# Kernel optimization log

Hardware: AMD Instinct MI355X
Metric: run time of the kernel (lower is better)

The kernel has to match this reference:

```python
import jax, jax.numpy as jnp
import numpy as np

B, C, T, H = 16, 128, 128, 128


def setup_inputs() -> dict:
    key = jax.random.key(0)
    ks = jax.random.split(key, 9)
    inp = {
        "food_relation": jax.random.normal(ks[0], (B, C, H), jnp.float32),
        "thorn_relation": jax.random.normal(ks[1], (B, C, T, H), jnp.float32),
        "clone": jax.random.normal(ks[2], (B, C, H), jnp.float32),
        "clone_relation": jax.random.normal(ks[3], (B, C, C, H), jnp.float32),
        "thorn_mask": jax.random.randint(ks[4], (B, T), 0, 2, jnp.int32),
        "clone_mask": jax.random.randint(ks[5], (B, C), 0, 2, jnp.int32),
        # MLP(layer_num=1) == Linear(in, h) + activation (ReLU)
        "W_thorn": jax.random.normal(ks[6], (2 * H, H), jnp.float32) / np.sqrt(2 * H),
        "b_thorn": jnp.zeros((H,), jnp.float32),
        "W_clone": jax.random.normal(ks[7], (3 * H, H), jnp.float32) / np.sqrt(3 * H),
        "b_clone": jnp.zeros((H,), jnp.float32),
        "W_agg": jax.random.normal(ks[8], (4 * H, H), jnp.float32) / np.sqrt(4 * H),
        "b_agg": jnp.zeros((H,), jnp.float32),
    }
    return inp


def reference(food_relation, thorn_relation, clone, clone_relation,
              thorn_mask, clone_mask,
              W_thorn, b_thorn, W_clone, b_clone, W_agg, b_agg):
    b, c, h = clone.shape
    t = thorn_relation.shape[2]
    tm = thorn_mask.astype(clone.dtype)[:, None, :, None]  # (b,1,t,1)
    cm = clone_mask.astype(clone.dtype)[:, None, :, None]  # (b,1,c,1)

    # thorn branch: MLP(concat([clone_i, thorn_rel_ij], -1))
    # == clone @ W[:h] (broadcast over t) + rel @ W[h:], avoiding the big concat
    x = ((clone @ W_thorn[:h])[:, :, None, :]
         + jnp.einsum('bcth,hk->bctk', thorn_relation, W_thorn[h:])
         + b_thorn)  # (b,c,t,h)
    thorn_agg = jnp.max(jax.nn.relu(x) * tm, axis=2)  # (b,c,h)

    # clone branch: MLP(concat([clone_i, clone_j, clone_rel_ij], -1))
    y = ((clone @ W_clone[:h])[:, :, None, :]
         + (clone @ W_clone[h:2 * h])[:, None, :, :]
         + jnp.einsum('bcdh,hk->bcdk', clone_relation, W_clone[2 * h:])
         + b_clone)  # (b,c,c,h)
    clone_agg = jnp.max(jax.nn.relu(y) * cm, axis=2)  # (b,c,h)

    agg = jnp.concatenate([clone, food_relation, thorn_agg, clone_agg], axis=-1)  # (b,c,4h)
    return clone + jax.nn.relu(agg @ W_agg + b_agg)
```

## Files before the change

kernel.cpp:

```cpp
#include <hip/hip_runtime.h>

#define BB 16
#define CC 128
#define TT 128
#define HH 128
#define BC (BB*CC)

typedef __attribute__((ext_vector_type(8))) short bf16x8;
typedef __attribute__((ext_vector_type(4))) float f32x4;

__device__ __forceinline__ unsigned short f2bf(float f) {
  union { float f; unsigned u; } v; v.f = f;
  unsigned u = v.u;
  u += 0x7FFFu + ((u >> 16) & 1u);
  return (unsigned short)(u >> 16);
}

__device__ __forceinline__ bf16x8 pack8(f32x4 a, f32x4 b) {
  bf16x8 r;
  r[0] = (short)f2bf(a[0]); r[1] = (short)f2bf(a[1]);
  r[2] = (short)f2bf(a[2]); r[3] = (short)f2bf(a[3]);
  r[4] = (short)f2bf(b[0]); r[5] = (short)f2bf(b[1]);
  r[6] = (short)f2bf(b[2]); r[7] = (short)f2bf(b[3]);
  return r;
}

__device__ __forceinline__ float bf2f(unsigned short u) {
  union { unsigned u; float f; } v; v.u = ((unsigned)u) << 16; return v.f;
}

__global__ __launch_bounds__(256) void prep_kernel(
    const float* __restrict__ Wt, const float* __restrict__ Wc, const float* __restrict__ Wa,
    const float* __restrict__ clone, const float* __restrict__ food,
    const float* __restrict__ bt, const float* __restrict__ bcl,
    const int* __restrict__ tmask, const int* __restrict__ cmask,
    unsigned short* __restrict__ W2sw, unsigned short* __restrict__ Wcsw,
    unsigned short* __restrict__ WaggT,
    float* __restrict__ cpt, float* __restrict__ cp1, float* __restrict__ cj2,
    unsigned short* __restrict__ agg,
    int* __restrict__ tidx, int* __restrict__ tcnt,
    int* __restrict__ cidx, int* __restrict__ ccnt) {
  const int blk = blockIdx.x, tid = threadIdx.x;
  if (blk < 48) {
    int i = blk * 256 + tid;
    if (i < 2048) {
      int f = i >> 6, l = i & 63;
      int kt = f >> 3, n = f & 7;
      int ncol = n * 16 + (l & 15);
      int k0 = kt * 32 + (l >> 4) * 8;
      unsigned short o[8];
      #pragma unroll
      for (int e = 0; e < 8; ++e) o[e] = f2bf(Wt[(128 + k0 + e) * 128 + ncol]);
      *(uint4*)&W2sw[i * 8] = *(uint4*)o;
    } else if (i < 4096) {
      int j = i - 2048;
      int f = j >> 6, l = j & 63;
      int kt = f >> 3, n = f & 7;
      int ncol = n * 16 + (l & 15);
      int k0 = kt * 32 + (l >> 4) * 8;
      unsigned short o[8];
      #pragma unroll
      for (int e = 0; e < 8; ++e) o[e] = f2bf(Wc[(256 + k0 + e) * 128 + ncol]);
      *(uint4*)&Wcsw[j * 8] = *(uint4*)o;
    } else {
      int j = i - 4096;
      int n = j >> 6, k0 = (j & 63) * 8;
      unsigned short o[8];
      #pragma unroll
      for (int e = 0; e < 8; ++e) o[e] = f2bf(Wa[(k0 + e) * 128 + n]);
      *(uint4*)&WaggT[n * 512 + k0] = *(uint4*)o;
    }
  } else if (blk < 304) {
    const int bc0 = (blk - 48) * 8;
    __shared__ float cl[8][128];
    for (int i = tid; i < 1024; i += 256) cl[i >> 7][i & 127] = clone[bc0 * 128 + i];
    __syncthreads();
    const int k = tid & 127, r0 = (tid >> 7) * 4;
    float s1[4], s2[4], s3[4];
    #pragma unroll
    for (int r = 0; r < 4; ++r) { s1[r] = bt[k]; s2[r] = bcl[k]; s3[r] = 0.f; }
    #pragma unroll 4
    for (int h = 0; h < 128; ++h) {
      float w1 = Wt[h * 128 + k], w2 = Wc[h * 128 + k], w3 = Wc[(128 + h) * 128 + k];
      #pragma unroll
      for (int r = 0; r < 4; ++r) {
        float c = cl[r0 + r][h];
        s1[r] = fmaf(c, w1, s1[r]);
        s2[r] = fmaf(c, w2, s2[r]);
        s3[r] = fmaf(c, w3, s3[r]);
      }
    }
    #pragma unroll
    for (int r = 0; r < 4; ++r) {
      cpt[(bc0 + r0 + r) * 128 + k] = s1[r];
      cp1[(bc0 + r0 + r) * 128 + k] = s2[r];
      cj2[(bc0 + r0 + r) * 128 + k] = s3[r];
    }
    for (int i = tid; i < 1024; i += 256) {
      int r = i >> 7, kk = i & 127;
      agg[(size_t)(bc0 + r) * 512 + kk]       = f2bf(cl[r][kk]);
      agg[(size_t)(bc0 + r) * 512 + 128 + kk] = f2bf(food[bc0 * 128 + i]);
    }
  } else {
    if (tid < 32) {
      int b = tid >> 1, which = tid & 1;
      const int* m = which ? cmask : tmask;
      int* idx = which ? cidx : tidx;
      int c = 0;
      for (int i = 0; i < 128; ++i)
        if (m[b * 128 + i]) idx[b * 128 + c++] = i;
      if (which) ccnt[b] = c; else tcnt[b] = c;
    }
  }
}

__global__ __launch_bounds__(512, 4) void branch9(
    const float* __restrict__ trel, const float* __restrict__ crel,
    const float* __restrict__ cpt, const float* __restrict__ cp1,
    const float* __restrict__ cj2,
    const int* __restrict__ tidx, const int* __restrict__ tcnt,
    const int* __restrict__ cidx, const int* __restrict__ ccnt,
    const uint4* __restrict__ W2sw, const uint4* __restrict__ Wcsw,
    unsigned short* __restrict__ agg) {
  __shared__ uint4 Wlds[32 * 64];
  __shared__ unsigned short cj2l[128][130];
  __shared__ float redbuf[2][8][128];
  __shared__ int idxl[128];
  __shared__ float biasl[8][128];

  const bool isClone = blockIdx.x < 256;
  const int tileIdx = blockIdx.x & 255;
  const float* __restrict__ rel     = isClone ? crel  : trel;
  const float* __restrict__ biasrow = isClone ? cp1   : cpt;
  const int*   __restrict__ idxg    = isClone ? cidx  : tidx;
  const uint4* __restrict__ Wsw     = isClone ? Wcsw  : W2sw;
  const int aggoff = isClone ? 384 : 256;

  const int tid = threadIdx.x;
  const int wave = tid >> 6, lane = tid & 63;
  const int l16 = lane & 15, lk = lane >> 4;
  const int bc0 = tileIdx << 3;
  const int b = bc0 >> 7;
  const int cnt = (isClone ? ccnt : tcnt)[b];
  const int cl  = cnt > 0 ? cnt : 1;
  const bool active = (wave * 16) < cnt;

  for (int i = tid; i < 2048; i += 512) Wlds[i] = Wsw[i];
  if (tid < 128) idxl[tid] = idxg[b * 128 + tid];
  #pragma unroll
  for (int i = 0; i < 2; ++i) {
    int q = i * 512 + tid;
    biasl[q >> 7][q & 127] = biasrow[bc0 * 128 + q];
  }
  if (isClone) {
    const float* cg = cj2 + (size_t)b * 128 * 128;
    for (int i = tid; i < 2048; i += 512) {
      int r = i >> 4, c8 = (i & 15) * 8;
      f32x4 a0 = *(const f32x4*)(cg + r * 128 + c8);
      f32x4 a1 = *(const f32x4*)(cg + r * 128 + c8 + 4);
      bf16x8 p = pack8(a0, a1);
      #pragma unroll
      for (int e = 0; e < 8; ++e) cj2l[c8 + e][r] = (unsigned short)p[e];
    }
  }
  __syncthreads();

  int rsel = wave * 16 + l16; if (rsel >= cl) rsel = cl - 1;
  const int row = active ? idxl[rsel] : 0;
  const float* R0 = rel + ((size_t)bc0 * 128 + row) * 128 + lk * 8;

  int rowj[4];
  if (isClone) {
    #pragma unroll
    for (int j = 0; j < 4; ++j) {
      int rs = wave * 16 + lk * 4 + j; if (rs >= cl) rs = cl - 1;
      rowj[j] = idxl[rs];
    }
  }

  f32x4 pf[4][2];
  if (active) {
    #pragma unroll
    for (int kt = 0; kt < 4; ++kt) {
      pf[kt][0] = *(const f32x4*)(R0 + kt * 32);
      pf[kt][1] = *(const f32x4*)(R0 + kt * 32 + 4);
    }
  }

  for (int t = 0; t < 8; ++t) {
    const int bc = bc0 + t;

    if (active) {
      bf16x8 afr[4];
      #pragma unroll
      for (int kt = 0; kt < 4; ++kt) afr[kt] = pack8(pf[kt][0], pf[kt][1]);

      if (t < 7) {
        const float* Rn = R0 + (size_t)(t + 1) * 16384;
        #pragma unroll
        for (int kt = 0; kt < 4; ++kt) {
          pf[kt][0] = *(const f32x4*)(Rn + kt * 32);
          pf[kt][1] = *(const f32x4*)(Rn + kt * 32 + 4);
        }
      }

      f32x4 acc[8];
      #pragma unroll
      for (int n = 0; n < 8; ++n) acc[n] = (f32x4){0.f, 0.f, 0.f, 0.f};
      #pragma unroll
      for (int kt = 0; kt < 4; ++kt) {
        #pragma unroll
        for (int n = 0; n < 8; ++n) {
          bf16x8 bfr = *(const bf16x8*)&Wlds[(kt * 8 + n) * 64 + lane];
          acc[n] = __builtin_amdgcn_mfma_f32_16x16x32_bf16(afr[kt], bfr, acc[n], 0, 0, 0);
        }
      }

      #pragma unroll
      for (int n = 0; n < 8; ++n) {
        const int col = n * 16 + l16;
        float bias = biasl[t][col];
        float m0 = 0.f;
        if (isClone) {
          #pragma unroll
          for (int j = 0; j < 4; ++j) {
            float x = acc[n][j] + bias + bf2f(cj2l[col][rowj[j]]);
            m0 = fmaxf(m0, fmaxf(x, 0.f));
          }
        } else {
          #pragma unroll
          for (int j = 0; j < 4; ++j)
            m0 = fmaxf(m0, fmaxf(acc[n][j] + bias, 0.f));
        }
        float v = fmaxf(m0, __shfl_xor(m0, 16));
        v = fmaxf(v, __shfl_xor(v, 32));
        if (lane < 16) redbuf[t & 1][wave][col] = v;
      }
    } else {
      if (lane < 16) {
        #pragma unroll
        for (int n = 0; n < 8; ++n) redbuf[t & 1][wave][n * 16 + lane] = 0.f;
      }
    }
    __syncthreads();
    if (tid < 128) {
      float v = redbuf[t & 1][0][tid];
      #pragma unroll
      for (int w2 = 1; w2 < 8; ++w2) v = fmaxf(v, redbuf[t & 1][w2][tid]);
      agg[(size_t)bc * 512 + aggoff + tid] = f2bf(v);
    }
  }
}

__global__ __launch_bounds__(256) void final_kernel(
    const unsigned short* __restrict__ agg, const unsigned short* __restrict__ WaggT,
    const float* __restrict__ clone, const float* __restrict__ bagg,
    float* __restrict__ out) {
  const int tid = threadIdx.x;
  const int wave = tid >> 6, lane = tid & 63;
  const int l16 = lane & 15, lk = lane >> 4;
  const int mrow = blockIdx.x * 16;

  f32x4 acc[2];
  acc[0] = (f32x4){0.f, 0.f, 0.f, 0.f};
  acc[1] = (f32x4){0.f, 0.f, 0.f, 0.f};
  #pragma unroll
  for (int kt = 0; kt < 16; ++kt) {
    bf16x8 a = *(const bf16x8*)(agg + (size_t)(mrow + l16) * 512 + kt * 32 + lk * 8);
    #pragma unroll
    for (int nn = 0; nn < 2; ++nn) {
      int ncol = (wave * 2 + nn) * 16 + l16;
      bf16x8 bfr = *(const bf16x8*)(WaggT + (size_t)ncol * 512 + kt * 32 + lk * 8);
      acc[nn] = __builtin_amdgcn_mfma_f32_16x16x32_bf16(a, bfr, acc[nn], 0, 0, 0);
    }
  }
  #pragma unroll
  for (int nn = 0; nn < 2; ++nn) {
    int col = (wave * 2 + nn) * 16 + l16;
    float bias = bagg[col];
    #pragma unroll
    for (int j = 0; j < 4; ++j) {
      int row = mrow + lk * 4 + j;
      out[row * 128 + col] = clone[row * 128 + col] + fmaxf(acc[nn][j] + bias, 0.f);
    }
  }
}

extern "C" void kernel_launch(void* const* d_in, const int* in_sizes, int n_in,
                              void* d_out, int out_size, void* d_ws, size_t ws_size,
                              hipStream_t stream) {
  const float* food  = (const float*)d_in[0];
  const float* trel  = (const float*)d_in[1];
  const float* clone = (const float*)d_in[2];
  const float* crel  = (const float*)d_in[3];
  const int*   tmask = (const int*)d_in[4];
  const int*   cmask = (const int*)d_in[5];
  const float* Wt    = (const float*)d_in[6];
  const float* bt    = (const float*)d_in[7];
  const float* Wc    = (const float*)d_in[8];
  const float* bcl   = (const float*)d_in[9];
  const float* Wa    = (const float*)d_in[10];
  const float* ba    = (const float*)d_in[11];
  float* out = (float*)d_out;

  char* w = (char*)d_ws;
  float* cpt = (float*)w;                      w += (size_t)BC * 128 * 4;
  float* cp1 = (float*)w;                      w += (size_t)BC * 128 * 4;
  float* cj2 = (float*)w;                      w += (size_t)BC * 128 * 4;
  unsigned short* W2sw  = (unsigned short*)w;  w += 32 * 64 * 8 * 2;
  unsigned short* Wcsw  = (unsigned short*)w;  w += 32 * 64 * 8 * 2;
  unsigned short* WaggT = (unsigned short*)w;  w += 128 * 512 * 2;
  unsigned short* aggb  = (unsigned short*)w;  w += (size_t)BC * 512 * 2;
  int* tidx = (int*)w;                         w += 16 * 128 * 4;
  int* cidx = (int*)w;                         w += 16 * 128 * 4;
  int* tcnt = (int*)w;                         w += 16 * 4;
  int* ccnt = (int*)w;                         w += 16 * 4;

  prep_kernel<<<305, 256, 0, stream>>>(Wt, Wc, Wa, clone, food, bt, bcl,
                                       tmask, cmask,
                                       W2sw, Wcsw, WaggT, cpt, cp1, cj2, aggb,
                                       tidx, tcnt, cidx, ccnt);
  branch9<<<512, 512, 0, stream>>>(trel, crel, cpt, cp1, cj2,
                                   tidx, tcnt, cidx, ccnt,
                                   (const uint4*)W2sw, (const uint4*)Wcsw, aggb);
  final_kernel<<<128, 256, 0, stream>>>(aggb, WaggT, clone, ba, out);
}
```

Baseline: 72.95 us.

## Assign one bc row per wave and loop over masked row groups

Each wave now owns one (b,c) pair and loops over groups of 16 masked rows, keeping a running max in registers, instead of all 8 waves splitting rows of the same bc and reducing through shared memory. This removes the per-step __syncthreads, the redbuf shared-memory reduction and the biasl staging. It also lets every wave do useful work regardless of mask count, where before waves past the count idled. The cost is a serial loop per wave whose length depends on the mask count, and row prefetch now covers only one group ahead.

```diff
diff --git a/kernel.cpp b/kernel.cpp
--- a/kernel.cpp
+++ b/kernel.cpp
@@ -114,7 +114,7 @@
   }
 }
 
-__global__ __launch_bounds__(512, 4) void branch9(
+__global__ __launch_bounds__(512, 4) void branch10(
     const float* __restrict__ trel, const float* __restrict__ crel,
     const float* __restrict__ cpt, const float* __restrict__ cp1,
     const float* __restrict__ cj2,
@@ -124,9 +124,7 @@
     unsigned short* __restrict__ agg) {
   __shared__ uint4 Wlds[32 * 64];
   __shared__ unsigned short cj2l[128][130];
-  __shared__ float redbuf[2][8][128];
   __shared__ int idxl[128];
-  __shared__ float biasl[8][128];
 
   const bool isClone = blockIdx.x < 256;
   const int tileIdx = blockIdx.x & 255;
@@ -143,15 +141,10 @@
   const int b = bc0 >> 7;
   const int cnt = (isClone ? ccnt : tcnt)[b];
   const int cl  = cnt > 0 ? cnt : 1;
-  const bool active = (wave * 16) < cnt;
+  const int G   = (cnt + 15) >> 4;
 
   for (int i = tid; i < 2048; i += 512) Wlds[i] = Wsw[i];
   if (tid < 128) idxl[tid] = idxg[b * 128 + tid];
-  #pragma unroll
-  for (int i = 0; i < 2; ++i) {
-    int q = i * 512 + tid;
-    biasl[q >> 7][q & 127] = biasrow[bc0 * 128 + q];
-  }
   if (isClone) {
     const float* cg = cj2 + (size_t)b * 128 * 128;
     for (int i = tid; i < 2048; i += 512) {
@@ -165,90 +158,88 @@
   }
   __syncthreads();
 
-  int rsel = wave * 16 + l16; if (rsel >= cl) rsel = cl - 1;
-  const int row = active ? idxl[rsel] : 0;
-  const float* R0 = rel + ((size_t)bc0 * 128 + row) * 128 + lk * 8;
-
-  int rowj[4];
-  if (isClone) {
-    #pragma unroll
-    for (int j = 0; j < 4; ++j) {
-      int rs = wave * 16 + lk * 4 + j; if (rs >= cl) rs = cl - 1;
-      rowj[j] = idxl[rs];
-    }
-  }
+  const int bc = bc0 + wave;
+  const float* Rb = rel + (size_t)bc * 16384 + lk * 8;
+
+  float bias[8];
+  #pragma unroll
+  for (int n = 0; n < 8; ++n) bias[n] = biasrow[bc * 128 + n * 16 + l16];
+
+  float vmax[8];
+  #pragma unroll
+  for (int n = 0; n < 8; ++n) vmax[n] = 0.f;
 
   f32x4 pf[4][2];
-  if (active) {
+  if (G > 0) {
+    int rs = l16 < cl ? l16 : cl - 1;
+    const float* Rt = Rb + idxl[rs] * 128;
     #pragma unroll
     for (int kt = 0; kt < 4; ++kt) {
-      pf[kt][0] = *(const f32x4*)(R0 + kt * 32);
-      pf[kt][1] = *(const f32x4*)(R0 + kt * 32 + 4);
-    }
-  }
-
-  for (int t = 0; t < 8; ++t) {
-    const int bc = bc0 + t;
-
-    if (active) {
-      bf16x8 afr[4];
-      #pragma unroll
-      for (int kt = 0; kt < 4; ++kt) afr[kt] = pack8(pf[kt][0], pf[kt][1]);
-
-      if (t < 7) {
-        const float* Rn = R0 + (size_t)(t + 1) * 16384;
-        #pragma unroll
-        for (int kt = 0; kt < 4; ++kt) {
-          pf[kt][0] = *(const f32x4*)(Rn + kt * 32);
-          pf[kt][1] = *(const f32x4*)(Rn + kt * 32 + 4);
-        }
-      }
-
-      f32x4 acc[8];
-      #pragma unroll
-      for (int n = 0; n < 8; ++n) acc[n] = (f32x4){0.f, 0.f, 0.f, 0.f};
+      pf[kt][0] = *(const f32x4*)(Rt + kt * 32);
+      pf[kt][1] = *(const f32x4*)(Rt + kt * 32 + 4);
+    }
+  }
+
+  for (int i = 0; i < G; ++i) {
+    bf16x8 afr[4];
+    #pragma unroll
+    for (int kt = 0; kt < 4; ++kt) afr[kt] = pack8(pf[kt][0], pf[kt][1]);
+
+    if (i + 1 < G) {
+      int rs = (i + 1) * 16 + l16; if (rs >= cl) rs = cl - 1;
+      const float* Rn = Rb + idxl[rs] * 128;
       #pragma unroll
       for (int kt = 0; kt < 4; ++kt) {
-        #pragma unroll
-        for (int n = 0; n < 8; ++n) {
-          bf16x8 bfr = *(const bf16x8*)&Wlds[(kt * 8 + n) * 64 + lane];
-          acc[n] = __builtin_amdgcn_mfma_f32_16x16x32_bf16(afr[kt], bfr, acc[n], 0, 0, 0);
-        }
-      }
-
+        pf[kt][0] = *(const f32x4*)(Rn + kt * 32);
+        pf[kt][1] = *(const f32x4*)(Rn + kt * 32 + 4);
+      }
+    }
+
+    f32x4 acc[8];
+    #pragma unroll
+    for (int n = 0; n < 8; ++n) acc[n] = (f32x4){0.f, 0.f, 0.f, 0.f};
+    #pragma unroll
+    for (int kt = 0; kt < 4; ++kt) {
+      #pragma unroll
+      for (int n = 0; n < 8; ++n) {
+        bf16x8 bfr = *(const bf16x8*)&Wlds[(kt * 8 + n) * 64 + lane];
+        acc[n] = __builtin_amdgcn_mfma_f32_16x16x32_bf16(afr[kt], bfr, acc[n], 0, 0, 0);
+      }
+    }
+
+    if (isClone) {
+      int rowj[4];
+      #pragma unroll
+      for (int j = 0; j < 4; ++j) {
+        int rs = i * 16 + lk * 4 + j; if (rs >= cl) rs = cl - 1;
+        rowj[j] = idxl[rs];
+      }
       #pragma unroll
       for (int n = 0; n < 8; ++n) {
         const int col = n * 16 + l16;
-        float bias = biasl[t][col];
-        float m0 = 0.f;
-        if (isClone) {
-          #pragma unroll
-          for (int j = 0; j < 4; ++j) {
-            float x = acc[n][j] + bias + bf2f(cj2l[col][rowj[j]]);
-            m0 = fmaxf(m0, fmaxf(x, 0.f));
-          }
-        } else {
-          #pragma unroll
-          for (int j = 0; j < 4; ++j)
-            m0 = fmaxf(m0, fmaxf(acc[n][j] + bias, 0.f));
+        #pragma unroll
+        for (int j = 0; j < 4; ++j) {
+          float x = acc[n][j] + bias[n] + bf2f(cj2l[col][rowj[j]]);
+          vmax[n] = fmaxf(vmax[n], fmaxf(x, 0.f));
         }
-        float v = fmaxf(m0, __shfl_xor(m0, 16));
-        v = fmaxf(v, __shfl_xor(v, 32));
-        if (lane < 16) redbuf[t & 1][wave][col] = v;
       }
     } else {
-      if (lane < 16) {
+      #pragma unroll
+      for (int n = 0; n < 8; ++n) {
         #pragma unroll
-        for (int n = 0; n < 8; ++n) redbuf[t & 1][wave][n * 16 + lane] = 0.f;
-      }
-    }
-    __syncthreads();
-    if (tid < 128) {
-      float v = redbuf[t & 1][0][tid];
-      #pragma unroll
-      for (int w2 = 1; w2 < 8; ++w2) v = fmaxf(v, redbuf[t & 1][w2][tid]);
-      agg[(size_t)bc * 512 + aggoff + tid] = f2bf(v);
-    }
+        for (int j = 0; j < 4; ++j)
+          vmax[n] = fmaxf(vmax[n], fmaxf(acc[n][j] + bias[n], 0.f));
+      }
+    }
+  }
+
+  unsigned short* aggw = agg + (size_t)bc * 512 + aggoff;
+  #pragma unroll
+  for (int n = 0; n < 8; ++n) {
+    float v = vmax[n];
+    v = fmaxf(v, __shfl_xor(v, 16));
+    v = fmaxf(v, __shfl_xor(v, 32));
+    if (lane < 16) aggw[n * 16 + lane] = f2bf(v);
   }
 }
 
@@ -320,8 +311,8 @@
                                        tmask, cmask,
                                        W2sw, Wcsw, WaggT, cpt, cp1, cj2, aggb,
                                        tidx, tcnt, cidx, ccnt);
-  branch9<<<512, 512, 0, stream>>>(trel, crel, cpt, cp1, cj2,
-                                   tidx, tcnt, cidx, ccnt,
-                                   (const uint4*)W2sw, (const uint4*)Wcsw, aggb);
+  branch10<<<512, 512, 0, stream>>>(trel, crel, cpt, cp1, cj2,
+                                    tidx, tcnt, cidx, ccnt,
+                                    (const uint4*)W2sw, (const uint4*)Wcsw, aggb);
   final_kernel<<<128, 256, 0, stream>>>(aggb, WaggT, clone, ba, out);
 }
```

New measurement: 168.5 us. +131.0%, slower.
